# Performance work log

Measured on AMD Instinct MI355X. Metric: run time of the kernel, lower is better.

## Reference

```python
import jax, jax.numpy as jnp
import numpy as np

L, H, R, N, E = 6, 128, 64, 10000, 160000
SSILU_SCALE = 1.0 / 0.6  # ScaledSiLU
INV_SQRT_3 = 1.0 / np.sqrt(3.0)
INV_SQRT_H = 1.0 / np.sqrt(H)
INV_SQRT_2 = 1.0 / np.sqrt(2.0)


def ssilu(x):
    return jax.nn.silu(x) * SSILU_SCALE


def lnorm(x, w, b):
    m = x.mean(-1, keepdims=True)
    v = jnp.var(x, axis=-1, keepdims=True)
    return (x - m) * jax.lax.rsqrt(v + 1e-5) * w + b


def gated_block(x, v, wv1, wv2, wu1, bu1, wu2, bu2, hout):
    # GatedEquivariantBlock: x [N,Hin], v [N,3,Hin]
    vec1 = jnp.linalg.norm(jnp.einsum('nci,io->nco', v, wv1), axis=-2)  # [N,Hin]
    vec2 = jnp.einsum('nci,io->nco', v, wv2)                            # [N,3,hout]
    h = ssilu(jnp.concatenate([x, vec1], -1) @ wu1 + bu1) @ wu2 + bu2   # [N,2*hout]
    xs, xv = h[..., :hout], h[..., hout:]
    return ssilu(xs), xv[:, None, :] * vec2


def forward_impl(edge_index, x, vec, edge_rbf, edge_vector,
                 ln_w, ln_b, xp1_w, xp1_b, xp2_w, xp2_b, rbf_w, rbf_b,
                 vp_w, xv1_w, xv1_b, xv2_w, xv2_b,
                 we1, be1, we2, be2,
                 g1_v1, g1_v2, g1_u1, g1_u1b, g1_u2, g1_u2b,
                 g2_v1, g2_v2, g2_u1, g2_u1b, g2_u2, g2_u2b):
    src, dst = edge_index[0], edge_index[1]  # message flows src(j) -> dst(i)
    for l in range(L):
        # ---- PaiNNMessage ----
        xh = ssilu(lnorm(x, ln_w[l], ln_b[l]) @ xp1_w[l] + xp1_b[l]) @ xp2_w[l] + xp2_b[l]  # [N,3H]
        rbfh = edge_rbf @ rbf_w[l] + rbf_b[l]                                                # [E,3H]
        m = xh[src] * rbfh                                                                    # gather + elementwise
        mx = m[:, :H]
        m2 = m[:, H:2 * H] * INV_SQRT_3
        m3 = m[:, 2 * H:]
        mvec = (vec[src] * m2[:, None, :] + m3[:, None, :] * edge_vector[:, :, None]) * INV_SQRT_H  # [E,3,H]
        dx = jax.ops.segment_sum(mx, dst, num_segments=N)
        dvec = jax.ops.segment_sum(mvec, dst, num_segments=N)
        x = (x + dx) * INV_SQRT_2
        vec = vec + dvec
        # ---- PaiNNUpdate ----
        vp = jnp.einsum('nci,io->nco', vec, vp_w[l])  # [N,3,2H]
        v1, v2 = vp[..., :H], vp[..., H:]
        vec_dot = (v1 * v2).sum(axis=1) * INV_SQRT_H  # [N,H]
        vnorm = jnp.sqrt((v2 ** 2).sum(axis=-2) + 1e-8)
        h = ssilu(jnp.concatenate([x, vnorm], -1) @ xv1_w[l] + xv1_b[l]) @ xv2_w[l] + xv2_b[l]  # [N,3H]
        xu1, xu2, xu3 = h[:, :H], h[:, H:2 * H], h[:, 2 * H:]
        x = x + (xu1 + xu2 * vec_dot) * INV_SQRT_2
        vec = vec + xu3[:, None, :] * v1
        # ScaleFactor is identity without a scale file
    energy = ssilu(x @ we1 + be1) @ we2 + be2  # [N,1] per-atom energy
    fx, fv = gated_block(x, vec, g1_v1, g1_v2, g1_u1, g1_u1b, g1_u2, g1_u2b, H // 2)
    fx, fv = gated_block(fx, fv, g2_v1, g2_v2, g2_u1, g2_u1b, g2_u2, g2_u2b, 1)
    forces = fv[..., 0]  # [N,3]
    return jnp.concatenate([energy, forces], axis=-1)  # [N,4] packed (energy, fx, fy, fz)


def setup_inputs() -> dict:
    key = jax.random.key(0)
    ks = iter(jax.random.split(key, 64))
    nrm = lambda shape, s=0.05: jax.random.normal(next(ks), shape, jnp.float32) * s
    return dict(
        x=jax.random.normal(next(ks), (N, H), jnp.float32),
        vec=jax.random.normal(next(ks), (N, 3, H), jnp.float32),
        edge_index=jax.random.randint(next(ks), (2, E), 0, N),
        edge_rbf=jax.random.uniform(next(ks), (E, R), jnp.float32),
        edge_vector=jax.random.normal(next(ks), (E, 3), jnp.float32),
        ln_w=jnp.ones((L, H)), ln_b=jnp.zeros((L, H)),
        xp1_w=nrm((L, H, H)), xp1_b=jnp.zeros((L, H)),
        xp2_w=nrm((L, H, 3 * H)), xp2_b=jnp.zeros((L, 3 * H)),
        rbf_w=nrm((L, R, 3 * H)), rbf_b=jnp.zeros((L, 3 * H)),
        vp_w=nrm((L, H, 2 * H)),
        xv1_w=nrm((L, 2 * H, H)), xv1_b=jnp.zeros((L, H)),
        xv2_w=nrm((L, H, 3 * H)), xv2_b=jnp.zeros((L, 3 * H)),
        we1=nrm((H, H // 2)), be1=jnp.zeros((H // 2,)),
        we2=nrm((H // 2, 1)), be2=jnp.zeros((1,)),
        g1_v1=nrm((H, H)), g1_v2=nrm((H, H // 2)),
        g1_u1=nrm((2 * H, H)), g1_u1b=jnp.zeros((H,)),
        g1_u2=nrm((H, H)), g1_u2b=jnp.zeros((H,)),
        g2_v1=nrm((H // 2, H // 2)), g2_v2=nrm((H // 2, 1)),
        g2_u1=nrm((H, H // 2)), g2_u1b=jnp.zeros((H // 2,)),
        g2_u2=nrm((H // 2, 2)), g2_u2b=jnp.zeros((2,)),
    )


def reference(x, vec, edge_index, edge_rbf, edge_vector,
              ln_w, ln_b, xp1_w, xp1_b, xp2_w, xp2_b, rbf_w, rbf_b,
              vp_w, xv1_w, xv1_b, xv2_w, xv2_b,
              we1, be1, we2, be2,
              g1_v1, g1_v2, g1_u1, g1_u1b, g1_u2, g1_u2b,
              g2_v1, g2_v2, g2_u1, g2_u1b, g2_u2, g2_u2b):
    return forward_impl(edge_index, x, vec, edge_rbf, edge_vector,
                        ln_w, ln_b, xp1_w, xp1_b, xp2_w, xp2_b, rbf_w, rbf_b,
                        vp_w, xv1_w, xv1_b, xv2_w, xv2_b,
                        we1, be1, we2, be2,
                        g1_v1, g1_v2, g1_u1, g1_u1b, g1_u2, g1_u2b,
                        g2_v1, g2_v2, g2_u1, g2_u1b, g2_u2, g2_u2b)
```

## Files before the change

### kernel.cpp

```cpp
#include <hip/hip_runtime.h>
#include <hip/hip_bf16.h>

#define NN 10000
#define EE 160000
#define LL 6

#define INV_SQRT_3f  0.57735026919f
#define INV_SQRT_Hf  0.08838834764832f
#define INV_SQRT_2f  0.70710678118655f

typedef _Float16 half8 __attribute__((ext_vector_type(8)));
typedef float f32x4 __attribute__((ext_vector_type(4)));

#define WE1OFF   0
#define WV1OFF   8192
#define WV2OFF   24576
#define WU1OFF   32768
#define WU2OFF   65536
#define G2V1OFF  81920
#define G2U1OFF  86016
#define WFIN_SZ  94208

__device__ __forceinline__ float ssilu_f(float v){
  float s = 1.0f / (1.0f + __expf(-v));
  return v * s * 1.6666666666667f;
}

__global__ __launch_bounds__(256) void k_hist(const int* __restrict__ edst, int* __restrict__ cnt){
  int i = blockIdx.x*256 + threadIdx.x;
  if (i < EE) atomicAdd(&cnt[edst[i]], 1);
}

__global__ __launch_bounds__(1024) void k_scan(const int* __restrict__ cnt,
                                               int* __restrict__ off, int* __restrict__ cur){
  __shared__ int ps[1024];
  int t = threadIdx.x;
  int base = t*10;
  int local[10];
  int s = 0;
  #pragma unroll
  for (int i=0;i<10;i++){
    int c = (base+i < NN) ? cnt[base+i] : 0;
    local[i] = s; s += c;
  }
  ps[t] = s;
  __syncthreads();
  for (int d=1; d<1024; d<<=1){
    int v = (t>=d) ? ps[t-d] : 0;
    __syncthreads();
    ps[t] += v;
    __syncthreads();
  }
  int pre = (t>0) ? ps[t-1] : 0;
  #pragma unroll
  for (int i=0;i<10;i++){
    int idx = base+i;
    if (idx < NN){ int o = pre + local[i]; off[idx]=o; cur[idx]=o; }
  }
  if (t==1023) off[NN] = ps[1023];
}

__global__ __launch_bounds__(256) void k_fill(const int* __restrict__ edst,
                                              int* __restrict__ cur, int* __restrict__ eord){
  int i = blockIdx.x*256 + threadIdx.x;
  if (i < EE){
    int d = edst[i];
    int p = atomicAdd(&cur[d], 1);
    eord[p] = i;
  }
}

__global__ __launch_bounds__(256) void k_sorta(const float* __restrict__ erbf,
                                               const int* __restrict__ eord, _Float16* __restrict__ eA){
  long i = (long)blockIdx.x*256 + threadIdx.x;
  if (i >= (long)EE*64) return;
  int j = i & 7, lane = (i >> 3) & 63, kh = (i >> 9) & 1;
  long tile = i >> 10;
  int e = eord[tile*16 + (lane&15)];
  eA[i] = (_Float16)erbf[(size_t)e*64 + kh*32 + (lane>>4)*8 + j];
}

__global__ __launch_bounds__(256) void k_sorte(const int* __restrict__ esrc, const float* __restrict__ evec,
                                               const int* __restrict__ eord, float4* __restrict__ es4){
  int p = blockIdx.x*256 + threadIdx.x;
  if (p >= EE) return;
  int e = eord[p];
  es4[p] = make_float4(evec[(size_t)e*3], evec[(size_t)e*3+1], evec[(size_t)e*3+2],
                       __int_as_float(esrc[e]));
}

__global__ __launch_bounds__(256) void k_packw(const float* __restrict__ w, _Float16* __restrict__ wf){
  int i = blockIdx.x*256 + threadIdx.x;
  if (i >= LL*24*2*64*8) return;
  int j    = i & 7;
  int lane = (i >> 3) & 63;
  int kh   = (i >> 9) & 1;
  int rest = i >> 10;
  int nb   = rest % 24;
  int l    = rest / 24;
  int k    = 32*kh + 8*(lane>>4) + j;
  int ch   = nb*16 + (lane&15);
  float v = w[((size_t)l*64 + k)*384 + ch];
  if (ch >= 128 && ch < 256) v *= INV_SQRT_3f;
  wf[i] = (_Float16)v;
}

__global__ __launch_bounds__(256) void k_packb(const float* __restrict__ b, float* __restrict__ bsc){
  int i = blockIdx.x*256 + threadIdx.x;
  if (i >= LL*384) return;
  int ch = i % 384;
  float v = b[i];
  if (ch >= 128 && ch < 256) v *= INV_SQRT_3f;
  bsc[i] = v;
}

struct PackTab {
  const float* s[40];
  _Float16* d[40];
  int K[40];
  int NO[40];
};
__global__ __launch_bounds__(256) void k_packall(PackTab tb){
  int e = blockIdx.y;
  int K = tb.K[e], NO = tb.NO[e];
  int tot = K*NO, KS = K >> 5;
  const float* s = tb.s[e];
  _Float16* d = tb.d[e];
  for (int i = blockIdx.x*256 + threadIdx.x; i < tot; i += gridDim.x*256){
    int j = i & 7, lane = (i >> 3) & 63, rest = i >> 9;
    int ks = rest % KS, nb = rest / KS;
    int k = ks*32 + (lane>>4)*8 + j, n = nb*16 + (lane&15);
    d[i] = (_Float16)s[(size_t)k*NO + n];
  }
}

__global__ __launch_bounds__(256) void k_cvt16(const float* __restrict__ v, _Float16* __restrict__ o, int n){
  int i = blockIdx.x*256 + threadIdx.x;
  if (i < n) o[i] = (_Float16)v[i];
}

__global__ __launch_bounds__(256) void k_xhgemm(
    const float* __restrict__ x,
    const float* __restrict__ lnw, const float* __restrict__ lnb,
    const _Float16* __restrict__ wf1, const float* __restrict__ b1,
    const _Float16* __restrict__ wf2, const float* __restrict__ b2,
    _Float16* __restrict__ xh16,
    const _Float16* __restrict__ eA, const _Float16* __restrict__ wf,
    const float* __restrict__ bsc, _Float16* __restrict__ rbfh)
{
  __shared__ _Float16 sA[32][136];
  __shared__ _Float16 sH[32][136];
  int t = threadIdx.x;
  if (blockIdx.x >= 313){
    int ob = (blockIdx.x - 313)*4 + (t >> 6);
    int lane = t & 63;
    int i0 = ob * 64;
    int tg = ob * 4;
    int ml = lane & 15, kg = lane >> 4;
    half8 a0[4], a1[4];
    #pragma unroll
    for (int tt = 0; tt < 4; tt++){
      a0[tt] = *(const half8*)(eA + ((size_t)((tg+tt)*2+0)*64 + lane)*8);
      a1[tt] = *(const half8*)(eA + ((size_t)((tg+tt)*2+1)*64 + lane)*8);
    }
    #pragma unroll 2
    for (int nb = 0; nb < 24; nb++){
      half8 b0 = *(const half8*)(wf + ((size_t)(nb*2+0)*64 + lane)*8);
      half8 b1h = *(const half8*)(wf + ((size_t)(nb*2+1)*64 + lane)*8);
      float bias = bsc[nb*16 + ml];
      #pragma unroll
      for (int tt = 0; tt < 4; tt++){
        f32x4 acc = {bias, bias, bias, bias};
        acc = __builtin_amdgcn_mfma_f32_16x16x32_f16(a0[tt], b0, acc, 0, 0, 0);
        acc = __builtin_amdgcn_mfma_f32_16x16x32_f16(a1[tt], b1h, acc, 0, 0, 0);
        _Float16* orow = rbfh + (size_t)(i0 + tt*16)*384 + nb*16 + ml;
        #pragma unroll
        for (int r = 0; r < 4; r++)
          orow[(size_t)(kg*4 + r)*384] = (_Float16)acc[r];
      }
    }
    return;
  }
  int n0 = blockIdx.x * 32;
  {
    int nd = t >> 3, sb = t & 7;
    int node = n0 + nd;
    float v[16];
    float s = 0.f, ss = 0.f;
    if (node < NN){
      const float* xr = x + (size_t)node*128 + sb*16;
      #pragma unroll
      for (int g = 0; g < 4; g++){
        float4 q = *(const float4*)(xr + g*4);
        v[g*4+0]=q.x; v[g*4+1]=q.y; v[g*4+2]=q.z; v[g*4+3]=q.w;
      }
      #pragma unroll
      for (int u = 0; u < 16; u++){ s += v[u]; ss += v[u]*v[u]; }
    } else {
      #pragma unroll
      for (int u = 0; u < 16; u++) v[u] = 0.f;
    }
    #pragma unroll
    for (int o2 = 4; o2 > 0; o2 >>= 1){
      s  += __shfl_xor(s, o2, 8);
      ss += __shfl_xor(ss, o2, 8);
    }
    float mean = s * (1.0f/128.0f);
    float var  = ss * (1.0f/128.0f) - mean*mean;
    float rstd = rsqrtf(var + 1e-5f);
    #pragma unroll
    for (int u = 0; u < 16; u++){
      int h = sb*16 + u;
      sA[nd][h] = (node < NN) ? (_Float16)((v[u]-mean)*rstd*lnw[h] + lnb[h]) : (_Float16)0.f;
    }
  }
  __syncthreads();
  int lane = t & 63, w = t >> 6, ml = lane & 15, kg = lane >> 4;
  int mt = w >> 1;
  {
    half8 a[4];
    #pragma unroll
    for (int ks = 0; ks < 4; ks++)
      a[ks] = *(const half8*)&sA[mt*16 + ml][ks*32 + kg*8];
    float hout[4][4];
    #pragma unroll
    for (int nb4 = 0; nb4 < 4; nb4++){
      int nb = (w&1)*4 + nb4;
      float bias = b1[nb*16 + ml];
      f32x4 acc = {bias, bias, bias, bias};
      #pragma unroll
      for (int ks = 0; ks < 4; ks++)
        acc = __builtin_amdgcn_mfma_f32_16x16x32_f16(a[ks],
                *(const half8*)(wf1 + ((size_t)(nb*4+ks)*64 + lane)*8), acc, 0,0,0);
      #pragma unroll
      for (int r = 0; r < 4; r++) hout[nb4][r] = ssilu_f(acc[r]);
    }
    #pragma unroll
    for (int nb4 = 0; nb4 < 4; nb4++){
      int nb = (w&1)*4 + nb4;
      #pragma unroll
      for (int r = 0; r < 4; r++)
        sH[mt*16 + kg*4 + r][nb*16 + ml] = (_Float16)hout[nb4][r];
    }
  }
  __syncthreads();
  {
    half8 a[4];
    #pragma unroll
    for (int ks = 0; ks < 4; ks++)
      a[ks] = *(const half8*)&sH[mt*16 + ml][ks*32 + kg*8];
    #pragma unroll 4
    for (int nb12 = 0; nb12 < 12; nb12++){
      int nb = (w&1)*12 + nb12;
      float bias = b2[nb*16 + ml];
      f32x4 acc = {bias, bias, bias, bias};
      #pragma unroll
      for (int ks = 0; ks < 4; ks++)
        acc = __builtin_amdgcn_mfma_f32_16x16x32_f16(a[ks],
                *(const half8*)(wf2 + ((size_t)(nb*4+ks)*64 + lane)*8), acc, 0,0,0);
      #pragma unroll
      for (int r = 0; r < 4; r++){
        int m = mt*16 + kg*4 + r;
        int node = n0 + m;
        if (node < NN) xh16[(size_t)node*384 + nb*16 + ml] = (_Float16)acc[r];
      }
    }
  }
}

__global__ __launch_bounds__(256) void k_edge3(
    const _Float16* __restrict__ rbfh,
    const float4* __restrict__ es4, const int* __restrict__ off,
    const _Float16* __restrict__ xh16, const _Float16* __restrict__ vec16,
    _Float16* __restrict__ dx, _Float16* __restrict__ dvec)
{
  int t = threadIdx.x;
  int lane = t & 63;
  int n = blockIdx.x*4 + (t>>6);
  if (n >= NN) return;
  int o0 = off[n], o1 = off[n+1];
  float ax0 = 0.f, ax1 = 0.f;
  float av00=0.f, av01=0.f, av10=0.f, av11=0.f, av20=0.f, av21=0.f;
  #pragma unroll 2
  for (int p = o0; p < o1; p++){
    const _Float16* hr = rbfh + (size_t)p*384;
    float h0 = (float)hr[lane];
    float h1 = (float)hr[64+lane];
    float h2 = (float)hr[128+lane];
    float h3 = (float)hr[192+lane];
    float h4 = (float)hr[256+lane];
    float h5 = (float)hr[320+lane];
    float4 q = es4[p];
    int sN = __float_as_int(q.w);
    const _Float16* xr = xh16 + (size_t)sN*384;
    float m0  = h0 * (float)xr[lane];
    float m1  = h1 * (float)xr[64+lane];
    float m2a = h2 * (float)xr[128+lane];
    float m2b = h3 * (float)xr[192+lane];
    float m3a = h4 * (float)xr[256+lane];
    float m3b = h5 * (float)xr[320+lane];
    ax0 += m0; ax1 += m1;
    const _Float16* vr = vec16 + (size_t)sN*384;
    av00 = fmaf((float)vr[lane],     m2a, av00); av00 = fmaf(m3a, q.x, av00);
    av01 = fmaf((float)vr[64+lane],  m2b, av01); av01 = fmaf(m3b, q.x, av01);
    av10 = fmaf((float)vr[128+lane], m2a, av10); av10 = fmaf(m3a, q.y, av10);
    av11 = fmaf((float)vr[192+lane], m2b, av11); av11 = fmaf(m3b, q.y, av11);
    av20 = fmaf((float)vr[256+lane], m2a, av20); av20 = fmaf(m3a, q.z, av20);
    av21 = fmaf((float)vr[320+lane], m2b, av21); av21 = fmaf(m3b, q.z, av21);
  }
  _Float16* dxr = dx + (size_t)n*128;
  dxr[lane] = (_Float16)ax0; dxr[64+lane] = (_Float16)ax1;
  _Float16* dvr = dvec + (size_t)n*384;
  dvr[lane]     = (_Float16)(av00 * INV_SQRT_Hf);
  dvr[64+lane]  = (_Float16)(av01 * INV_SQRT_Hf);
  dvr[128+lane] = (_Float16)(av10 * INV_SQRT_Hf);
  dvr[192+lane] = (_Float16)(av11 * INV_SQRT_Hf);
  dvr[256+lane] = (_Float16)(av20 * INV_SQRT_Hf);
  dvr[320+lane] = (_Float16)(av21 * INV_SQRT_Hf);
}

__global__ __launch_bounds__(256) void k_node_mfma(
    float* __restrict__ xbuf, float* __restrict__ vbuf,
    const _Float16* __restrict__ dx, const _Float16* __restrict__ dvec,
    const _Float16* __restrict__ wfvp,
    const _Float16* __restrict__ wfxv1, const float* __restrict__ xv1_b,
    const _Float16* __restrict__ wfxv2, const float* __restrict__ xv2_b,
    _Float16* __restrict__ vec16)
{
  __shared__ _Float16 sV1[96][136];
  __shared__ _Float16 sCat[32][264];
  __shared__ _Float16 sVD[32][128];
  int t = threadIdx.x;
  int n0 = blockIdx.x * 32;
  int lane = t & 63, w = t >> 6, ml = lane & 15, kg = lane >> 4;
  int mt = w & 1, nbb = (w >> 1) * 4;
  float vd[4][4], vn[4][4];
  #pragma unroll
  for (int i=0;i<4;i++){
    #pragma unroll
    for (int r=0;r<4;r++){ vd[i][r]=0.f; vn[i][r]=0.f; }
  }
  int arow = n0 + mt*16 + ml;
  bool aok = arow < NN;
  for (int cd = 0; cd < 3; cd++){
    half8 a[4];
    #pragma unroll
    for (int ks = 0; ks < 4; ks++){
      if (aok){
        const float* vr = vbuf + (size_t)arow*384 + cd*128 + ks*32 + kg*8;
        const _Float16* dr = dvec + (size_t)arow*384 + cd*128 + ks*32 + kg*8;
        float4 q0 = *(const float4*)(vr);
        float4 q1 = *(const float4*)(vr+4);
        half8 dh = *(const half8*)(dr);
        a[ks][0]=(_Float16)(q0.x+(float)dh[0]); a[ks][1]=(_Float16)(q0.y+(float)dh[1]);
        a[ks][2]=(_Float16)(q0.z+(float)dh[2]); a[ks][3]=(_Float16)(q0.w+(float)dh[3]);
        a[ks][4]=(_Float16)(q1.x+(float)dh[4]); a[ks][5]=(_Float16)(q1.y+(float)dh[5]);
        a[ks][6]=(_Float16)(q1.z+(float)dh[6]); a[ks][7]=(_Float16)(q1.w+(float)dh[7]);
      } else {
        #pragma unroll
        for (int j=0;j<8;j++) a[ks][j] = (_Float16)0.f;
      }
    }
    #pragma unroll
    for (int nb4 = 0; nb4 < 4; nb4++){
      int nb1 = nbb + nb4;
      f32x4 acc1 = {0.f,0.f,0.f,0.f}, acc2 = {0.f,0.f,0.f,0.f};
      #pragma unroll
      for (int ks = 0; ks < 4; ks++){
        acc1 = __builtin_amdgcn_mfma_f32_16x16x32_f16(a[ks],
                 *(const half8*)(wfvp + ((size_t)(nb1*4+ks)*64 + lane)*8), acc1, 0,0,0);
        acc2 = __builtin_amdgcn_mfma_f32_16x16x32_f16(a[ks],
                 *(const half8*)(wfvp + ((size_t)((nb1+8)*4+ks)*64 + lane)*8), acc2, 0,0,0);
      }
      #pragma unroll
      for (int r = 0; r < 4; r++){
        float v1v = acc1[r], v2v = acc2[r];
        vd[nb4][r] += v1v*v2v;
        vn[nb4][r] += v2v*v2v;
        sV1[cd*32 + mt*16 + kg*4 + r][nb1*16 + ml] = (_Float16)v1v;
      }
    }
  }
  #pragma unroll
  for (int nb4 = 0; nb4 < 4; nb4++){
    #pragma unroll
    for (int r = 0; r < 4; r++){
      int m = mt*16 + kg*4 + r, c = (nbb+nb4)*16 + ml;
      sVD[m][c] = (_Float16)(vd[nb4][r] * INV_SQRT_Hf);
      sCat[m][128 + c] = (_Float16)sqrtf(vn[nb4][r] + 1e-8f);
    }
  }
  {
    int nd = t >> 3, sb = t & 7;
    int node = n0 + nd;
    if (node < NN){
      const float* xr = xbuf + (size_t)node*128 + sb*16;
      const _Float16* dr = dx + (size_t)node*128 + sb*16;
      half8 da = *(const half8*)(dr);
      half8 db = *(const half8*)(dr+8);
      #pragma unroll
      for (int g = 0; g < 4; g++){
        float4 qa = *(const float4*)(xr + g*4);
        float d0 = (float)((g<2)?da[g*4+0]:db[(g-2)*4+0]);
        float d1 = (float)((g<2)?da[g*4+1]:db[(g-2)*4+1]);
        float d2 = (float)((g<2)?da[g*4+2]:db[(g-2)*4+2]);
        float d3 = (float)((g<2)?da[g*4+3]:db[(g-2)*4+3]);
        sCat[nd][sb*16+g*4+0] = (_Float16)((qa.x+d0)*INV_SQRT_2f);
        sCat[nd][sb*16+g*4+1] = (_Float16)((qa.y+d1)*INV_SQRT_2f);
        sCat[nd][sb*16+g*4+2] = (_Float16)((qa.z+d2)*INV_SQRT_2f);
        sCat[nd][sb*16+g*4+3] = (_Float16)((qa.w+d3)*INV_SQRT_2f);
      }
    } else {
      #pragma unroll
      for (int u = 0; u < 16; u++) sCat[nd][sb*16+u] = (_Float16)0.f;
    }
  }
  __syncthreads();
  float hreg[4][4];
  {
    half8 a[8];
    #pragma unroll
    for (int ks = 0; ks < 8; ks++)
      a[ks] = *(const half8*)&sCat[mt*16 + ml][ks*32 + kg*8];
    #pragma unroll
    for (int nb4 = 0; nb4 < 4; nb4++){
      int nb = (w>>1)*4 + nb4;
      float bias = xv1_b[nb*16 + ml];
      f32x4 acc = {bias, bias, bias, bias};
      #pragma unroll
      for (int ks = 0; ks < 8; ks++)
        acc = __builtin_amdgcn_mfma_f32_16x16x32_f16(a[ks],
                *(const half8*)(wfxv1 + ((size_t)(nb*8+ks)*64 + lane)*8), acc, 0,0,0);
      #pragma unroll
      for (int r = 0; r < 4; r++) hreg[nb4][r] = ssilu_f(acc[r]);
    }
  }
  __syncthreads();
  #pragma unroll
  for (int nb4 = 0; nb4 < 4; nb4++){
    int nb = (w>>1)*4 + nb4;
    #pragma unroll
    for (int r = 0; r < 4; r++)
      sCat[mt*16 + kg*4 + r][nb*16 + ml] = (_Float16)hreg[nb4][r];
  }
  __syncthreads();
  {
    half8 a[4];
    #pragma unroll
    for (int ks = 0; ks < 4; ks++)
      a[ks] = *(const half8*)&sCat[mt*16 + ml][ks*32 + kg*8];
    #pragma unroll 2
    for (int nb4 = 0; nb4 < 4; nb4++){
      int nbu = nbb + nb4;
      float b1v = xv2_b[nbu*16 + ml];
      float b2v = xv2_b[(nbu+8)*16 + ml];
      float b3v = xv2_b[(nbu+16)*16 + ml];
      f32x4 au1 = {b1v,b1v,b1v,b1v};
      f32x4 au2 = {b2v,b2v,b2v,b2v};
      f32x4 au3 = {b3v,b3v,b3v,b3v};
      #pragma unroll
      for (int ks = 0; ks < 4; ks++){
        au1 = __builtin_amdgcn_mfma_f32_16x16x32_f16(a[ks],
                *(const half8*)(wfxv2 + ((size_t)(nbu*4+ks)*64 + lane)*8), au1, 0,0,0);
        au2 = __builtin_amdgcn_mfma_f32_16x16x32_f16(a[ks],
                *(const half8*)(wfxv2 + ((size_t)((nbu+8)*4+ks)*64 + lane)*8), au2, 0,0,0);
        au3 = __builtin_amdgcn_mfma_f32_16x16x32_f16(a[ks],
                *(const half8*)(wfxv2 + ((size_t)((nbu+16)*4+ks)*64 + lane)*8), au3, 0,0,0);
      }
      #pragma unroll
      for (int r = 0; r < 4; r++){
        int m = mt*16 + kg*4 + r;
        int node = n0 + m;
        if (node >= NN) continue;
        int c = nbu*16 + ml;
        float xu1 = au1[r], xu2 = au2[r], xu3 = au3[r];
        float vdv = (float)sVD[m][c];
        size_t px = (size_t)node*128 + c;
        float xn = (xbuf[px] + (float)dx[px]) * INV_SQRT_2f;
        xbuf[px] = xn + (xu1 + xu2*vdv) * INV_SQRT_2f;
        #pragma unroll
        for (int cd = 0; cd < 3; cd++){
          float v1v = (float)sV1[cd*32 + m][c];
          size_t pv = (size_t)node*384 + cd*128 + c;
          float vo = vbuf[pv] + (float)dvec[pv] + xu3*v1v;
          vbuf[pv] = vo;
          vec16[pv] = (_Float16)vo;
        }
      }
    }
  }
}

__global__ __launch_bounds__(256) void k_final(
    const float* __restrict__ x, const float* __restrict__ vec,
    const _Float16* __restrict__ wfin,
    const float* __restrict__ be1, const float* __restrict__ we2, const float* __restrict__ be2,
    const float* __restrict__ u1b, const float* __restrict__ u2b,
    const float* __restrict__ g2v2, const float* __restrict__ g2u1b, const float* __restrict__ g2u2,
    const float* __restrict__ g2u2b,
    float* __restrict__ out)
{
  __shared__ _Float16 sCat[32][264];
  __shared__ _Float16 sV2[3][32][72];
  __shared__ _Float16 sH[32][136];
  __shared__ _Float16 sFV[3][32][72];
  __shared__ _Float16 sE1[32][72];
  __shared__ float sR[3][32];
  int t = threadIdx.x;
  int n0 = blockIdx.x * 32;
  int lane = t & 63, w = t >> 6, ml = lane & 15, kg = lane >> 4;
  int mt = w & 1, nh = w >> 1;

  {
    int nd = t >> 3, sb = t & 7;
    int node = n0 + nd;
    if (node < NN){
      const float* xr = x + (size_t)node*128 + sb*16;
      #pragma unroll
      for (int g = 0; g < 4; g++){
        float4 q = *(const float4*)(xr + g*4);
        sCat[nd][sb*16+g*4+0]=(_Float16)q.x; sCat[nd][sb*16+g*4+1]=(_Float16)q.y;
        sCat[nd][sb*16+g*4+2]=(_Float16)q.z; sCat[nd][sb*16+g*4+3]=(_Float16)q.w;
      }
    } else {
      #pragma unroll
      for (int u = 0; u < 16; u++) sCat[nd][sb*16+u] = (_Float16)0.f;
    }
  }
  {
    int arow = n0 + mt*16 + ml;
    bool aok = arow < NN;
    float n1sq[4][4];
    #pragma unroll
    for (int i=0;i<4;i++){
      #pragma unroll
      for (int r=0;r<4;r++) n1sq[i][r]=0.f;
    }
    for (int cd = 0; cd < 3; cd++){
      half8 a[4];
      #pragma unroll
      for (int ks = 0; ks < 4; ks++){
        if (aok){
          const float* vr = vec + (size_t)arow*384 + cd*128 + ks*32 + kg*8;
          float4 q0 = *(const float4*)(vr);
          float4 q1 = *(const float4*)(vr+4);
          a[ks][0]=(_Float16)q0.x; a[ks][1]=(_Float16)q0.y; a[ks][2]=(_Float16)q0.z; a[ks][3]=(_Float16)q0.w;
          a[ks][4]=(_Float16)q1.x; a[ks][5]=(_Float16)q1.y; a[ks][6]=(_Float16)q1.z; a[ks][7]=(_Float16)q1.w;
        } else {
          #pragma unroll
          for (int j=0;j<8;j++) a[ks][j] = (_Float16)0.f;
        }
      }
      #pragma unroll
      for (int nb4 = 0; nb4 < 4; nb4++){
        int nb = nh*4 + nb4;
        f32x4 acc = {0.f,0.f,0.f,0.f};
        #pragma unroll
        for (int ks = 0; ks < 4; ks++)
          acc = __builtin_amdgcn_mfma_f32_16x16x32_f16(a[ks],
                  *(const half8*)(wfin + WV1OFF + ((size_t)(nb*4+ks)*64 + lane)*8), acc, 0,0,0);
        #pragma unroll
        for (int r = 0; r < 4; r++) n1sq[nb4][r] += acc[r]*acc[r];
      }
      #pragma unroll
      for (int q = 0; q < 2; q++){
        int nb = nh*2 + q;
        f32x4 acc = {0.f,0.f,0.f,0.f};
        #pragma unroll
        for (int ks = 0; ks < 4; ks++)
          acc = __builtin_amdgcn_mfma_f32_16x16x32_f16(a[ks],
                  *(const half8*)(wfin + WV2OFF + ((size_t)(nb*4+ks)*64 + lane)*8), acc, 0,0,0);
        #pragma unroll
        for (int r = 0; r < 4; r++)
          sV2[cd][mt*16 + kg*4 + r][nb*16 + ml] = (_Float16)acc[r];
      }
    }
    #pragma unroll
    for (int nb4 = 0; nb4 < 4; nb4++){
      #pragma unroll
      for (int r = 0; r < 4; r++)
        sCat[mt*16 + kg*4 + r][128 + nh*64 + nb4*16 + ml] = (_Float16)sqrtf(n1sq[nb4][r]);
    }
  }
  __syncthreads();
  {
    half8 a[8];
    #pragma unroll
    for (int ks = 0; ks < 8; ks++)
      a[ks] = *(const half8*)&sCat[mt*16 + ml][ks*32 + kg*8];
    #pragma unroll
    for (int q = 0; q < 2; q++){
      int nb = nh*2 + q;
      float bias = be1[nb*16 + ml];
      f32x4 acc = {bias, bias, bias, bias};
      #pragma unroll
      for (int ks = 0; ks < 4; ks++)
        acc = __builtin_amdgcn_mfma_f32_16x16x32_f16(a[ks],
                *(const half8*)(wfin + WE1OFF + ((size_t)(nb*4+ks)*64 + lane)*8), acc, 0,0,0);
      #pragma unroll
      for (int r = 0; r < 4; r++)
        sE1[mt*16 + kg*4 + r][nb*16 + ml] = (_Float16)ssilu_f(acc[r]);
    }
    #pragma unroll
    for (int nb4 = 0; nb4 < 4; nb4++){
      int nb = nh*4 + nb4;
      float bias = u1b[nb*16 + ml];
      f32x4 acc = {bias, bias, bias, bias};
      #pragma unroll
      for (int ks = 0; ks < 8; ks++)
        acc = __builtin_amdgcn_mfma_f32_16x16x32_f16(a[ks],
                *(const half8*)(wfin + WU1OFF + ((size_t)(nb*8+ks)*64 + lane)*8), acc, 0,0,0);
      #pragma unroll
      for (int r = 0; r < 4; r++)
        sH[mt*16 + kg*4 + r][nb*16 + ml] = (_Float16)ssilu_f(acc[r]);
    }
  }
  __syncthreads();
  {
    half8 a[4];
    #pragma unroll
    for (int ks = 0; ks < 4; ks++)
      a[ks] = *(const half8*)&sH[mt*16 + ml][ks*32 + kg*8];
    #pragma unroll
    for (int nb4 = 0; nb4 < 4; nb4++){
      int nb = nh*4 + nb4;
      float bias = u2b[nb*16 + ml];
      f32x4 acc = {bias, bias, bias, bias};
      #pragma unroll
      for (int ks = 0; ks < 4; ks++)
        acc = __builtin_amdgcn_mfma_f32_16x16x32_f16(a[ks],
                *(const half8*)(wfin + WU2OFF + ((size_t)(nb*4+ks)*64 + lane)*8), acc, 0,0,0);
      int c = nb*16 + ml;
      #pragma unroll
      for (int r = 0; r < 4; r++){
        int m = mt*16 + kg*4 + r;
        if (c < 64){
          sCat[m][c] = (_Float16)ssilu_f(acc[r]);
        } else {
          float xv = acc[r];
          #pragma unroll
          for (int cd = 0; cd < 3; cd++)
            sFV[cd][m][c-64] = (_Float16)(xv * (float)sV2[cd][m][c-64]);
        }
      }
    }
    float wev = we2[lane];
    #pragma unroll
    for (int i = 0; i < 8; i++){
      int nd = w*8 + i;
      float v = (float)sE1[nd][lane] * wev;
      #pragma unroll
      for (int o2 = 32; o2 > 0; o2 >>= 1) v += __shfl_xor(v, o2, 64);
      int node = n0 + nd;
      if (lane == 0 && node < NN) out[(size_t)node*4 + 0] = v + be2[0];
    }
  }
  __syncthreads();
  {
    float n1sq[2][4];
    #pragma unroll
    for (int q=0;q<2;q++){
      #pragma unroll
      for (int r=0;r<4;r++) n1sq[q][r]=0.f;
    }
    for (int cd = 0; cd < 3; cd++){
      half8 a[2];
      #pragma unroll
      for (int ks = 0; ks < 2; ks++)
        a[ks] = *(const half8*)&sFV[cd][mt*16 + ml][ks*32 + kg*8];
      #pragma unroll
      for (int q = 0; q < 2; q++){
        int nb = nh*2 + q;
        f32x4 acc = {0.f,0.f,0.f,0.f};
        #pragma unroll
        for (int ks = 0; ks < 2; ks++)
          acc = __builtin_amdgcn_mfma_f32_16x16x32_f16(a[ks],
                  *(const half8*)(wfin + G2V1OFF + ((size_t)(nb*2+ks)*64 + lane)*8), acc, 0,0,0);
        #pragma unroll
        for (int r = 0; r < 4; r++) n1sq[q][r] += acc[r]*acc[r];
      }
    }
    #pragma unroll
    for (int q = 0; q < 2; q++){
      #pragma unroll
      for (int r = 0; r < 4; r++)
        sCat[mt*16 + kg*4 + r][64 + (nh*2+q)*16 + ml] = (_Float16)sqrtf(n1sq[q][r]);
    }
    float g2v = g2v2[lane];
    #pragma unroll
    for (int i = 0; i < 8; i++){
      int nd = w*8 + i;
      #pragma unroll
      for (int cd = 0; cd < 3; cd++){
        float v = (float)sFV[cd][nd][lane] * g2v;
        #pragma unroll
        for (int o2 = 32; o2 > 0; o2 >>= 1) v += __shfl_xor(v, o2, 64);
        if (lane == 0) sR[cd][nd] = v;
      }
    }
  }
  __syncthreads();
  {
    half8 a[4];
    #pragma unroll
    for (int ks = 0; ks < 4; ks++)
      a[ks] = *(const half8*)&sCat[mt*16 + ml][ks*32 + kg*8];
    #pragma unroll
    for (int q = 0; q < 2; q++){
      int nb = nh*2 + q;
      float bias = g2u1b[nb*16 + ml];
      f32x4 acc = {bias, bias, bias, bias};
      #pragma unroll
      for (int ks = 0; ks < 4; ks++)
        acc = __builtin_amdgcn_mfma_f32_16x16x32_f16(a[ks],
                *(const half8*)(wfin + G2U1OFF + ((size_t)(nb*4+ks)*64 + lane)*8), acc, 0,0,0);
      #pragma unroll
      for (int r = 0; r < 4; r++)
        sE1[mt*16 + kg*4 + r][nb*16 + ml] = (_Float16)ssilu_f(acc[r]);
    }
  }
  __syncthreads();
  {
    float g2w = g2u2[lane*2 + 1];
    #pragma unroll
    for (int i = 0; i < 8; i++){
      int nd = w*8 + i;
      float v = (float)sE1[nd][lane] * g2w;
      #pragma unroll
      for (int o2 = 32; o2 > 0; o2 >>= 1) v += __shfl_xor(v, o2, 64);
      int node = n0 + nd;
      if (lane == 0 && node < NN){
        float h21 = v + g2u2b[1];
        out[(size_t)node*4 + 1] = h21 * sR[0][nd];
        out[(size_t)node*4 + 2] = h21 * sR[1][nd];
        out[(size_t)node*4 + 3] = h21 * sR[2][nd];
      }
    }
  }
}

extern "C" void kernel_launch(void* const* d_in, const int* in_sizes, int n_in,
                              void* d_out, int out_size, void* d_ws, size_t ws_size,
                              hipStream_t stream)
{
  const float* x_in   = (const float*)d_in[0];
  const float* vec_in = (const float*)d_in[1];
  const int*   eidx   = (const int*)d_in[2];
  const float* erbf   = (const float*)d_in[3];
  const float* evec   = (const float*)d_in[4];
  const float* ln_w  = (const float*)d_in[5];
  const float* ln_b  = (const float*)d_in[6];
  const float* xp1_w = (const float*)d_in[7];
  const float* xp1_b = (const float*)d_in[8];
  const float* xp2_w = (const float*)d_in[9];
  const float* xp2_b = (const float*)d_in[10];
  const float* rbf_w = (const float*)d_in[11];
  const float* rbf_b = (const float*)d_in[12];
  const float* vp_w  = (const float*)d_in[13];
  const float* xv1_w = (const float*)d_in[14];
  const float* xv1_b = (const float*)d_in[15];
  const float* xv2_w = (const float*)d_in[16];
  const float* xv2_b = (const float*)d_in[17];
  const float* we1 = (const float*)d_in[18];
  const float* be1 = (const float*)d_in[19];
  const float* we2 = (const float*)d_in[20];
  const float* be2 = (const float*)d_in[21];
  const float* g1_v1 = (const float*)d_in[22];
  const float* g1_v2 = (const float*)d_in[23];
  const float* g1_u1 = (const float*)d_in[24];
  const float* g1_u1b = (const float*)d_in[25];
  const float* g1_u2 = (const float*)d_in[26];
  const float* g1_u2b = (const float*)d_in[27];
  const float* g2_v1 = (const float*)d_in[28];
  const float* g2_v2 = (const float*)d_in[29];
  const float* g2_u1 = (const float*)d_in[30];
  const float* g2_u1b = (const float*)d_in[31];
  const float* g2_u2 = (const float*)d_in[32];
  const float* g2_u2b = (const float*)d_in[33];
  float* out = (float*)d_out;

  char* base = (char*)d_ws;
  size_t o = 0;
  auto alloc = [&](size_t bytes) -> char* {
    char* p = base + o;
    o = (o + bytes + 255) & ~(size_t)255;
    return p;
  };
  float* x_cur   = (float*)alloc((size_t)NN*128*4);
  float* vec_cur = (float*)alloc((size_t)NN*384*4);
  _Float16* dx   = (_Float16*)alloc((size_t)NN*128*2);
  _Float16* dvec = (_Float16*)alloc((size_t)NN*384*2);
  _Float16* xh16 = (_Float16*)alloc((size_t)NN*384*2);
  _Float16* vec16= (_Float16*)alloc((size_t)NN*384*2);
  int*   eord    = (int*)alloc((size_t)EE*4);
  int*   off     = (int*)alloc((size_t)(NN+1)*4);
  _Float16* wf   = (_Float16*)alloc((size_t)LL*24576*2);
  float* bsc     = (float*)alloc((size_t)LL*384*4);
  _Float16* wfn  = (_Float16*)alloc((size_t)LL*180224*2);
  _Float16* wfin = (_Float16*)alloc((size_t)WFIN_SZ*2);
  _Float16* eA   = (_Float16*)alloc((size_t)EE*64*2);
  float4* es4    = (float4*)alloc((size_t)EE*16);
  _Float16* rbfh = (_Float16*)alloc((size_t)EE*384*2);
  int* cnt = (int*)dx;
  int* cur = cnt + NN;

  hipMemcpyAsync(x_cur, x_in, sizeof(float)*(size_t)NN*128, hipMemcpyDeviceToDevice, stream);
  hipMemcpyAsync(vec_cur, vec_in, sizeof(float)*(size_t)NN*384, hipMemcpyDeviceToDevice, stream);

  const int* esrc = eidx;
  const int* edst = eidx + EE;

  hipMemsetAsync(cnt, 0, sizeof(int)*NN, stream);
  k_hist<<<(EE+255)/256, 256, 0, stream>>>(edst, cnt);
  k_scan<<<1, 1024, 0, stream>>>(cnt, off, cur);
  k_fill<<<(EE+255)/256, 256, 0, stream>>>(edst, cur, eord);
  k_sorta<<<(EE*64+255)/256, 256, 0, stream>>>(erbf, eord, eA);
  k_sorte<<<(EE+255)/256, 256, 0, stream>>>(esrc, evec, eord, es4);
  k_packw<<<(LL*24576+255)/256, 256, 0, stream>>>(rbf_w, wf);
  k_packb<<<(LL*384+255)/256, 256, 0, stream>>>(rbf_b, bsc);
  k_cvt16<<<(NN*384+255)/256, 256, 0, stream>>>(vec_in, vec16, NN*384);

  {
    PackTab tb;
    for (int l = 0; l < LL; l++){
      _Float16* wb = wfn + (size_t)l*180224;
      tb.s[l*5+0] = xp1_w + (size_t)l*128*128; tb.d[l*5+0] = wb;          tb.K[l*5+0]=128; tb.NO[l*5+0]=128;
      tb.s[l*5+1] = xp2_w + (size_t)l*128*384; tb.d[l*5+1] = wb+16384;    tb.K[l*5+1]=128; tb.NO[l*5+1]=384;
      tb.s[l*5+2] = vp_w  + (size_t)l*128*256; tb.d[l*5+2] = wb+65536;    tb.K[l*5+2]=128; tb.NO[l*5+2]=256;
      tb.s[l*5+3] = xv1_w + (size_t)l*256*128; tb.d[l*5+3] = wb+98304;    tb.K[l*5+3]=256; tb.NO[l*5+3]=128;
      tb.s[l*5+4] = xv2_w + (size_t)l*128*384; tb.d[l*5+4] = wb+131072;   tb.K[l*5+4]=128; tb.NO[l*5+4]=384;
    }
    tb.s[30] = we1;   tb.d[30] = wfin + WE1OFF;  tb.K[30]=128; tb.NO[30]=64;
    tb.s[31] = g1_v1; tb.d[31] = wfin + WV1OFF;  tb.K[31]=128; tb.NO[31]=128;
    tb.s[32] = g1_v2; tb.d[32] = wfin + WV2OFF;  tb.K[32]=128; tb.NO[32]=64;
    tb.s[33] = g1_u1; tb.d[33] = wfin + WU1OFF;  tb.K[33]=256; tb.NO[33]=128;
    tb.s[34] = g1_u2; tb.d[34] = wfin + WU2OFF;  tb.K[34]=128; tb.NO[34]=128;
    tb.s[35] = g2_v1; tb.d[35] = wfin + G2V1OFF; tb.K[35]=64;  tb.NO[35]=64;
    tb.s[36] = g2_u1; tb.d[36] = wfin + G2U1OFF; tb.K[36]=128; tb.NO[36]=64;
    k_packall<<<dim3(24, 37), 256, 0, stream>>>(tb);
  }

  for (int l = 0; l < LL; l++){
    _Float16* wb = wfn + (size_t)l*180224;
    k_xhgemm<<<938, 256, 0, stream>>>(x_cur, ln_w + l*128, ln_b + l*128,
        wb, xp1_b + l*128, wb+16384, xp2_b + l*384, xh16,
        eA, wf + (size_t)l*24576, bsc + (size_t)l*384, rbfh);
    k_edge3<<<NN/4, 256, 0, stream>>>(rbfh, es4, off, xh16, vec16, dx, dvec);
    k_node_mfma<<<(NN+31)/32, 256, 0, stream>>>(x_cur, vec_cur, dx, dvec,
        wb+65536, wb+98304, xv1_b + l*128, wb+131072, xv2_b + l*384, vec16);
  }
  k_final<<<(NN+31)/32, 256, 0, stream>>>(x_cur, vec_cur, wfin,
      be1, we2, be2, g1_u1b, g1_u2b, g2_v2, g2_u1b, g2_u2, g2_u2b, out);
}
```

Before: 888.7 us.

## Interleave xh and vec fp16 rows per node, keep node-kernel intermediates in registers

```diff
diff --git a/kernel.cpp b/kernel.cpp
--- a/kernel.cpp
+++ b/kernel.cpp
@@ -134,9 +134,11 @@
   }
 }
 
-__global__ __launch_bounds__(256) void k_cvt16(const float* __restrict__ v, _Float16* __restrict__ o, int n){
+__global__ __launch_bounds__(256) void k_cvt16v(const float* __restrict__ v, _Float16* __restrict__ xv){
   int i = blockIdx.x*256 + threadIdx.x;
-  if (i < n) o[i] = (_Float16)v[i];
+  if (i >= NN*384) return;
+  int node = i / 384, r = i % 384;
+  xv[(size_t)node*768 + 384 + r] = (_Float16)v[i];
 }
 
 __global__ __launch_bounds__(256) void k_xhgemm(
@@ -144,7 +146,7 @@
     const float* __restrict__ lnw, const float* __restrict__ lnb,
     const _Float16* __restrict__ wf1, const float* __restrict__ b1,
     const _Float16* __restrict__ wf2, const float* __restrict__ b2,
-    _Float16* __restrict__ xh16,
+    _Float16* __restrict__ xv16,
     const _Float16* __restrict__ eA, const _Float16* __restrict__ wf,
     const float* __restrict__ bsc, _Float16* __restrict__ rbfh)
 {
@@ -262,7 +264,7 @@
       for (int r = 0; r < 4; r++){
         int m = mt*16 + kg*4 + r;
         int node = n0 + m;
-        if (node < NN) xh16[(size_t)node*384 + nb*16 + ml] = (_Float16)acc[r];
+        if (node < NN) xv16[(size_t)node*768 + nb*16 + ml] = (_Float16)acc[r];
       }
     }
   }
@@ -271,7 +273,7 @@
 __global__ __launch_bounds__(256) void k_edge3(
     const _Float16* __restrict__ rbfh,
     const float4* __restrict__ es4, const int* __restrict__ off,
-    const _Float16* __restrict__ xh16, const _Float16* __restrict__ vec16,
+    const _Float16* __restrict__ xv16,
     _Float16* __restrict__ dx, _Float16* __restrict__ dvec)
 {
   int t = threadIdx.x;
@@ -292,7 +294,7 @@
     float h5 = (float)hr[320+lane];
     float4 q = es4[p];
     int sN = __float_as_int(q.w);
-    const _Float16* xr = xh16 + (size_t)sN*384;
+    const _Float16* xr = xv16 + (size_t)sN*768;
     float m0  = h0 * (float)xr[lane];
     float m1  = h1 * (float)xr[64+lane];
     float m2a = h2 * (float)xr[128+lane];
@@ -300,7 +302,7 @@
     float m3a = h4 * (float)xr[256+lane];
     float m3b = h5 * (float)xr[320+lane];
     ax0 += m0; ax1 += m1;
-    const _Float16* vr = vec16 + (size_t)sN*384;
+    const _Float16* vr = xr + 384;
     av00 = fmaf((float)vr[lane],     m2a, av00); av00 = fmaf(m3a, q.x, av00);
     av01 = fmaf((float)vr[64+lane],  m2b, av01); av01 = fmaf(m3b, q.x, av01);
     av10 = fmaf((float)vr[128+lane], m2a, av10); av10 = fmaf(m3a, q.y, av10);
@@ -325,23 +327,24 @@
     const _Float16* __restrict__ wfvp,
     const _Float16* __restrict__ wfxv1, const float* __restrict__ xv1_b,
     const _Float16* __restrict__ wfxv2, const float* __restrict__ xv2_b,
-    _Float16* __restrict__ vec16)
+    _Float16* __restrict__ xv16)
 {
-  __shared__ _Float16 sV1[96][136];
   __shared__ _Float16 sCat[32][264];
-  __shared__ _Float16 sVD[32][128];
   int t = threadIdx.x;
   int n0 = blockIdx.x * 32;
   int lane = t & 63, w = t >> 6, ml = lane & 15, kg = lane >> 4;
   int mt = w & 1, nbb = (w >> 1) * 4;
-  float vd[4][4], vn[4][4];
+  float v1g[3][4][4];
+  float vdg[4][4];
+  float vn[4][4];
   #pragma unroll
   for (int i=0;i<4;i++){
     #pragma unroll
-    for (int r=0;r<4;r++){ vd[i][r]=0.f; vn[i][r]=0.f; }
+    for (int r=0;r<4;r++){ vdg[i][r]=0.f; vn[i][r]=0.f; }
   }
   int arow = n0 + mt*16 + ml;
   bool aok = arow < NN;
+  #pragma unroll
   for (int cd = 0; cd < 3; cd++){
     half8 a[4];
     #pragma unroll
@@ -375,9 +378,9 @@
       #pragma unroll
       for (int r = 0; r < 4; r++){
         float v1v = acc1[r], v2v = acc2[r];
-        vd[nb4][r] += v1v*v2v;
+        vdg[nb4][r] += v1v*v2v;
         vn[nb4][r] += v2v*v2v;
-        sV1[cd*32 + mt*16 + kg*4 + r][nb1*16 + ml] = (_Float16)v1v;
+        v1g[cd][nb4][r] = v1v;
       }
     }
   }
@@ -386,7 +389,7 @@
     #pragma unroll
     for (int r = 0; r < 4; r++){
       int m = mt*16 + kg*4 + r, c = (nbb+nb4)*16 + ml;
-      sVD[m][c] = (_Float16)(vd[nb4][r] * INV_SQRT_Hf);
+      vdg[nb4][r] *= INV_SQRT_Hf;
       sCat[m][128 + c] = (_Float16)sqrtf(vn[nb4][r] + 1e-8f);
     }
   }
@@ -474,17 +477,17 @@
         if (node >= NN) continue;
         int c = nbu*16 + ml;
         float xu1 = au1[r], xu2 = au2[r], xu3 = au3[r];
-        float vdv = (float)sVD[m][c];
+        float vdv = vdg[nb4][r];
         size_t px = (size_t)node*128 + c;
         float xn = (xbuf[px] + (float)dx[px]) * INV_SQRT_2f;
         xbuf[px] = xn + (xu1 + xu2*vdv) * INV_SQRT_2f;
         #pragma unroll
         for (int cd = 0; cd < 3; cd++){
-          float v1v = (float)sV1[cd*32 + m][c];
+          float v1v = v1g[cd][nb4][r];
           size_t pv = (size_t)node*384 + cd*128 + c;
           float vo = vbuf[pv] + (float)dvec[pv] + xu3*v1v;
           vbuf[pv] = vo;
-          vec16[pv] = (_Float16)vo;
+          xv16[(size_t)node*768 + 384 + cd*128 + c] = (_Float16)vo;
         }
       }
     }
@@ -790,8 +793,7 @@
   float* vec_cur = (float*)alloc((size_t)NN*384*4);
   _Float16* dx   = (_Float16*)alloc((size_t)NN*128*2);
   _Float16* dvec = (_Float16*)alloc((size_t)NN*384*2);
-  _Float16* xh16 = (_Float16*)alloc((size_t)NN*384*2);
-  _Float16* vec16= (_Float16*)alloc((size_t)NN*384*2);
+  _Float16* xv16 = (_Float16*)alloc((size_t)NN*768*2);
   int*   eord    = (int*)alloc((size_t)EE*4);
   int*   off     = (int*)alloc((size_t)(NN+1)*4);
   _Float16* wf   = (_Float16*)alloc((size_t)LL*24576*2);
@@ -818,7 +820,7 @@
   k_sorte<<<(EE+255)/256, 256, 0, stream>>>(esrc, evec, eord, es4);
   k_packw<<<(LL*24576+255)/256, 256, 0, stream>>>(rbf_w, wf);
   k_packb<<<(LL*384+255)/256, 256, 0, stream>>>(rbf_b, bsc);
-  k_cvt16<<<(NN*384+255)/256, 256, 0, stream>>>(vec_in, vec16, NN*384);
+  k_cvt16v<<<(NN*384+255)/256, 256, 0, stream>>>(vec_in, xv16);
 
   {
     PackTab tb;
@@ -843,11 +845,11 @@
   for (int l = 0; l < LL; l++){
     _Float16* wb = wfn + (size_t)l*180224;
     k_xhgemm<<<938, 256, 0, stream>>>(x_cur, ln_w + l*128, ln_b + l*128,
-        wb, xp1_b + l*128, wb+16384, xp2_b + l*384, xh16,
+        wb, xp1_b + l*128, wb+16384, xp2_b + l*384, xv16,
         eA, wf + (size_t)l*24576, bsc + (size_t)l*384, rbfh);
-    k_edge3<<<NN/4, 256, 0, stream>>>(rbfh, es4, off, xh16, vec16, dx, dvec);
+    k_edge3<<<NN/4, 256, 0, stream>>>(rbfh, es4, off, xv16, dx, dvec);
     k_node_mfma<<<(NN+31)/32, 256, 0, stream>>>(x_cur, vec_cur, dx, dvec,
-        wb+65536, wb+98304, xv1_b + l*128, wb+131072, xv2_b + l*384, vec16);
+        wb+65536, wb+98304, xv1_b + l*128, wb+131072, xv2_b + l*384, xv16);
   }
   k_final<<<(NN+31)/32, 256, 0, stream>>>(x_cur, vec_cur, wfin,
       be1, we2, be2, g1_u1b, g1_u2b, g2_v2, g2_u1b, g2_u2, g2_u2b, out);
```

New measurement: 905.9 us. Within noise of the previous version (+1.9%).
